# Kernel optimization log

Measured on AMD Instinct MI355X. Metric: run time of the kernel, lower is better.

The kernel has to match this reference:

```python
import jax, jax.numpy as jnp
from jax import lax
import numpy as np
from functools import partial

B, C, H, W = 4, 3, 256, 256
HW = H * W
KCAP = 32          # max tracked components per (batch, class) slot
MAX_ITER = 5
KSIZE = 5


def _depthwise_sum(x, k):
    c = x.shape[1]
    w = jnp.ones((c, 1, k, k), x.dtype)
    return lax.conv_general_dilated(x, w, (1, 1), [(k // 2, k // 2)] * 2,
                                    feature_group_count=c,
                                    dimension_numbers=('NCHW', 'OIHW', 'NCHW'))


def erode(x):
    return (_depthwise_sum(x, KSIZE) >= KSIZE * KSIZE - 0.5).astype(x.dtype)


def dilate(x):
    return (_depthwise_sum(x, KSIZE) > 0.5).astype(x.dtype)


def _maxpool3_int(L):
    return lax.reduce_window(L, jnp.int32(0), lax.max, (1, 1, 3, 3), (1, 1, 1, 1),
                             [(0, 0), (0, 0), (1, 1), (1, 1)])


def label_cc(binary):
    # connected-component labeling by iterated 3x3 max-pool of pixel indices,
    # exactly as find_components_max_pool (labels = max flat pixel index in comp)
    b = lax.stop_gradient(binary) > 0.5
    idx = jnp.arange(HW, dtype=jnp.int32).reshape(1, 1, H, W)
    L0 = jnp.where(b, idx, 0)

    def cond(st):
        return st[1]

    def body(st):
        L, _ = st
        Ln = jnp.where(b, _maxpool3_int(L), 0)
        return Ln, jnp.any(Ln != L)

    L, _ = lax.while_loop(cond, body, (L0, jnp.array(True)))
    return L


def extract_components(Lf, binf):
    # per (b,c): top-KCAP components sorted by comp.sum() = size*label/maxL (desc)
    flat = Lf.reshape(-1)
    sizes = jnp.zeros((HW,), jnp.float32).at[flat].add(binf.reshape(-1))
    idx = jnp.arange(HW, dtype=jnp.int32)
    is_root = (flat == idx) & (flat > 0)  # label 0 excluded, as in torch code
    key = jnp.where(is_root, lax.stop_gradient(sizes) * idx.astype(jnp.float32), -1.0)
    _, top_lab = lax.top_k(key, KCAP)
    valid = key[top_lab] > 0.0
    maxL = jnp.maximum(flat.max(), 1).astype(jnp.float32)
    v = top_lab.astype(jnp.float32)
    s = jnp.where(valid, sizes[top_lab] * v / maxL, 0.0)  # comp.sum()
    lab = jnp.where(valid, top_lab, -1)
    # component tensor = mask * label/maxL, exactly mask*L/max(L) of the original
    comps = (Lf[None] == lab[:, None, None]).astype(jnp.float32) * (v / maxL)[:, None, None]
    return s, comps, valid


def process_step(P, n, bar, s, comps, valid, t):
    # overlaps vs components stored BEFORE this step; new comps within a step
    # are pixel-disjoint so they can never match each other (overlap == 0).
    OV = jnp.einsum('jhw,khw->jk', comps, P)

    def body(carry, inp):
        P, n, bar = carry
        s_j, comp_j, valid_j, ov_j = inp
        best = jnp.argmax(ov_j)
        matched = ov_j[best] > 0.0
        widx = jnp.clip(jnp.where(matched, best, n), 0, KCAP - 1)
        can = valid_j & (matched | (n < KCAP))
        bar = bar.at[widx, t].set(jnp.where(can, s_j, bar[widx, t]))
        add = valid_j & (~matched) & (n < KCAP)
        nw = jnp.minimum(n, KCAP - 1)
        P = P.at[nw].set(jnp.where(add, comp_j, P[nw]))
        return (P, n + add.astype(n.dtype), bar), None

    (P, n, bar), _ = lax.scan(body, (P, n, bar), (s, comps, valid, OV))
    return P, n, bar


def compute_barcodes(binary):
    half = MAX_ITER // 2
    seq = [(binary, half)]
    m = binary
    for t in range(half):
        m = erode(m)
        seq.append((m, half + t + 1))
    m = binary
    for t in range(half):
        m = dilate(m)
        seq.append((m, half - t - 1))
    BC = B * C
    P = jnp.zeros((BC, KCAP, H, W), jnp.float32)
    n = jnp.zeros((BC,), jnp.int32)
    bar = jnp.zeros((BC, KCAP, MAX_ITER), jnp.float32)
    for mp, t in seq:  # fixed 5-step schedule (structural loop)
        L = label_cc(mp).reshape(BC, H, W)
        s, comps, valid = jax.vmap(extract_components)(L, mp.reshape(BC, H, W))
        P, n, bar = jax.vmap(partial(process_step, t=t))(P, n, bar, s, comps, valid)
    return bar.reshape(B, C, KCAP, MAX_ITER), n.reshape(B, C)


def topo_forward(predictions, gumbel, targets):
    y_soft = jax.nn.softmax(predictions + gumbel, axis=1)
    hard = jax.nn.one_hot(jnp.argmax(y_soft, axis=1), C, axis=1, dtype=jnp.float32)
    binary_pred = hard + y_soft - lax.stop_gradient(y_soft)  # straight-through
    binary_tgt = jnp.moveaxis(jax.nn.one_hot(targets, C, dtype=jnp.float32), -1, 1)
    bp, n_p = compute_barcodes(binary_pred)
    bt, n_t = compute_barcodes(binary_tgt)
    k = jnp.arange(KCAP)
    valid_p = k[None, None] < n_p[:, :, None]
    has_t = k[None, None] < n_t[:, :, None]
    pmax = bp.max(-1)
    pmax = jnp.where(pmax > 0, pmax, 1.0)
    tgt = jnp.where(has_t[..., None], bt, 0.0)
    term = jnp.sum((tgt - bp) ** 2, -1) / pmax ** 2
    losses = jnp.sum(jnp.where(valid_p, term, 0.0), axis=(1, 2))
    return losses.mean()  # reduction='mean'


def setup_inputs() -> dict:
    key = jax.random.key(0)
    k1, k2, k3 = jax.random.split(key, 3)
    # blob-like logits: low-res noise upsampled so component counts stay < KCAP
    lo = jax.random.normal(k1, (B, C, 16, 16), jnp.float32)
    predictions = 8.0 * jax.image.resize(lo, (B, C, H, W), 'linear')
    lo_t = jax.random.normal(k2, (B, C, 16, 16), jnp.float32)
    targets = jnp.argmax(jax.image.resize(lo_t, (B, C, H, W), 'linear'), axis=1).astype(jnp.int32)
    u = jax.random.uniform(k3, (B, C, H, W), jnp.float32, minval=1e-6, maxval=1.0 - 1e-6)
    gumbel = -jnp.log(-jnp.log(u))  # standard Gumbel noise (F.gumbel_softmax)
    return {"predictions": predictions, "gumbel": gumbel, "targets": targets}


def reference(predictions, gumbel, targets):
    return topo_forward(predictions, gumbel, targets)
```

## Files before the change

kernel.cpp:

```cpp
#include <hip/hip_runtime.h>

#define NB 4
#define NC 3
#define BC 12
#define HW 65536
#define KCAP 32
#define MAXI 5
#define RUNCAP 16384
#define NSLOT 120
#define NCH 24

typedef unsigned long long u64;
typedef unsigned int u32;

__device__ __forceinline__ int uf_find(int* P, int x){
  while (true){
    int p = P[x];
    if (p == x) return x;
    int gp = P[p];
    if (gp == p) return p;
    P[x] = gp;
    x = gp;
  }
}
__device__ __forceinline__ void uf_union_max(int* P, int a, int b){
  while (true){
    a = uf_find(P, a); b = uf_find(P, b);
    if (a == b) return;
    if (a > b){ int t = a; a = b; b = t; }
    int old = atomicCAS(&P[a], a, b);
    if (old == a) return;
    a = old;
  }
}

template<typename F>
__device__ __forceinline__ void walk_runs(const u64* wv, F&& emit){
  int open_s = -1;
  #pragma unroll
  for (int wi = 0; wi < 4; wi++){
    u64 v = wv[wi];
    int base = wi << 6;
    int pos = 0;
    while (pos < 64){
      u64 rem = v >> pos;
      if (open_s >= 0){
        u64 nz = ~rem;
        int z = nz ? __builtin_ctzll(nz) : 64;
        if (z >= 64 - pos){ pos = 64; }
        else { emit(open_s, base + pos + z); open_s = -1; pos += z; }
      } else {
        if (rem == 0ull){ pos = 64; }
        else {
          int o = __builtin_ctzll(rem);
          open_s = base + pos + o;
          pos += o;
        }
      }
    }
  }
  if (open_s >= 0) emit(open_s, 256);
}

__global__ void k_bin(const float* __restrict__ pred, const float* __restrict__ gum,
                      const int* __restrict__ tgt, u64* __restrict__ bmAll){
  int g = blockIdx.x * 256 + threadIdx.x;
  int b = g >> 16, p = g & (HW - 1);
  size_t base = (size_t)b * NC * HW + p;
  float v0 = pred[base]        + gum[base];
  float v1 = pred[base + HW]   + gum[base + HW];
  float v2 = pred[base + 2*HW] + gum[base + 2*HW];
  int a = 0; float m = v0;
  if (v1 > m){ m = v1; a = 1; }
  if (v2 > m){ m = v2; a = 2; }
  int tg = tgt[(size_t)b * HW + p];
  u64 p0 = __ballot(a == 0), p1 = __ballot(a == 1), p2 = __ballot(a == 2);
  u64 t0 = __ballot(tg == 0), t1 = __ballot(tg == 1), t2 = __ballot(tg == 2);
  if ((threadIdx.x & 63) == 0){
    int w = p >> 6;
    int sp = b * NC;
    bmAll[(size_t)(sp + 0) * 1024 + w] = p0;
    bmAll[(size_t)(sp + 1) * 1024 + w] = p1;
    bmAll[(size_t)(sp + 2) * 1024 + w] = p2;
    int st = 60 + b * NC;
    bmAll[(size_t)(st + 0) * 1024 + w] = t0;
    bmAll[(size_t)(st + 1) * 1024 + w] = t1;
    bmAll[(size_t)(st + 2) * 1024 + w] = t2;
  }
}

__global__ void k_morph4(const u64* __restrict__ bmAll, u64* __restrict__ bmAllW,
                         int4 srcs, int4 dsts, int4 flgs){
  int t = blockIdx.x * 256 + threadIdx.x;
  int job = t / 12288, rest = t % 12288;
  int s = rest >> 10, word = rest & 1023;
  int row = word >> 2, w = word & 3;
  int srcG = job == 0 ? srcs.x : job == 1 ? srcs.y : job == 2 ? srcs.z : srcs.w;
  int dstG = job == 0 ? dsts.x : job == 1 ? dsts.y : job == 2 ? dsts.z : dsts.w;
  int er   = job == 0 ? flgs.x : job == 1 ? flgs.y : job == 2 ? flgs.z : flgs.w;
  const u64* bs = bmAll + (size_t)(srcG * BC + s) * 1024;
  u64 res = er ? ~0ull : 0ull;
  for (int dy = -2; dy <= 2; dy++){
    int y = row + dy;
    if (y < 0 || y > 255){ if (er) res = 0; continue; }
    const u64* rw = bs + y * 4;
    u64 m = rw[w];
    u64 l = (w > 0) ? rw[w-1] : 0ull;
    u64 r = (w < 3) ? rw[w+1] : 0ull;
    u64 x1l = (m << 1) | (l >> 63);
    u64 x2l = (m << 2) | (l >> 62);
    u64 x1r = (m >> 1) | (r << 63);
    u64 x2r = (m >> 2) | (r << 62);
    u64 h = er ? (m & x1l & x2l & x1r & x2r) : (m | x1l | x2l | x1r | x2r);
    res = er ? (res & h) : (res | h);
  }
  bmAllW[(size_t)(dstG * BC + s) * 1024 + word] = res;
}

__global__ __launch_bounds__(1024) void k_cc_runs(
    const u64* __restrict__ bmAll, u32* __restrict__ selRuns,
    int* __restrict__ selCnt, float* __restrict__ sSel, float* __restrict__ scaleSel){
  __shared__ int par[RUNCAP];
  __shared__ u32 pkz[RUNCAP];
  __shared__ int rs[257];
  __shared__ u64 wcand[16*KCAP];
  __shared__ u64 selKeys[KCAP];
  __shared__ int selRoot[KCAP];
  __shared__ int wsum[4], wsum2[4];
  __shared__ int lmS;
  int u = blockIdx.x, t = threadIdx.x;
  int lane = t & 63, wid = t >> 6;
  bool rowT = t < 256;
  u64 wv[4] = {0,0,0,0};
  int nr = 0;
  if (rowT){
    const u64* bp = bmAll + (size_t)u * 1024 + t * 4;
    #pragma unroll
    for (int i = 0; i < 4; i++) wv[i] = bp[i];
    walk_runs(wv, [&](int a, int b){ (void)a; (void)b; nr++; });
  }
  if (t == 0) lmS = 0;
  {
    int v = nr;
    #pragma unroll
    for (int d = 1; d < 64; d <<= 1){
      int o = __shfl_up(v, d);
      if (lane >= d) v += o;
    }
    if (rowT && lane == 63) wsum[wid] = v;
    __syncthreads();
    if (rowT){
      int pre = 0;
      for (int q = 0; q < wid; q++) pre += wsum[q];
      rs[t] = pre + v - nr;
      if (t == 255) rs[256] = pre + v;
    }
    __syncthreads();
  }
  int NR = rs[256];
  int NRc = NR < RUNCAP ? NR : RUNCAP;
  int myBase = rowT ? rs[t] : 0;
  for (int i = t; i < NRc; i += 1024) par[i] = i;
  if (rowT){
    int o = myBase;
    walk_runs(wv, [&](int a, int b){
      if (o < RUNCAP) pkz[o] = ((u32)t << 16) | ((u32)a << 8) | (u32)(b - 1);
      o++;
    });
  }
  __syncthreads();
  for (int i = t; i < NRc; i += 1024){
    u32 v = pkz[i];
    int r = v >> 16;
    if (r == 0) continue;
    int s2 = (int)((v >> 8) & 255), E2 = (int)(v & 255);
    int a0 = rs[r-1], a1 = rs[r];
    if (a1 > NRc) a1 = NRc;
    if (a0 >= a1) continue;
    int lo = a0, hi = a1;
    while (lo < hi){
      int mid = (lo + hi) >> 1;
      if ((int)(pkz[mid] & 255) >= s2 - 1) hi = mid; else lo = mid + 1;
    }
    for (int j = lo; j < a1; j++){
      int s1 = (int)((pkz[j] >> 8) & 255);
      if (s1 > E2 + 1) break;
      uf_union_max(par, i, j);
    }
  }
  __syncthreads();
  for (int i = t; i < NRc; i += 1024){
    int r = i, p = par[r];
    while (p != r){ r = p; p = par[r]; }
    par[i] = r;
  }
  __syncthreads();
  {
    int lm = 0;
    for (int i = t; i < NRc; i += 1024){
      u32 v = pkz[i];
      int s0 = (int)((v >> 8) & 255), E = (int)(v & 255);
      atomicAdd(&par[par[i] & 16383], (E - s0 + 1) << 14);
      lm = max(lm, (int)(v >> 16) * 256 + E);
    }
    #pragma unroll
    for (int off = 32; off > 0; off >>= 1) lm = max(lm, __shfl_xor(lm, off));
    if (lane == 0) atomicMax(&lmS, lm);
  }
  __syncthreads();
  float maxLf = (float)(lmS >= 1 ? lmS : 1);
  for (int i = t; i < NRc; i += 1024){
    int pv = par[i];
    if ((pv & 16383) == i){
      u32 v = pkz[i];
      int lab = (int)(v >> 16) * 256 + (int)(v & 255);
      if (lab > 0){
        float key = (float)((u32)pv >> 14) * (float)lab;
        pkz[i] = __float_as_uint(key);
        par[i] = (lab << 14) | i;
      } else {
        pkz[i] = 0;
      }
    }
  }
  __syncthreads();
  {
    u64 myBest = 0;
    for (int i = t; i < NRc; i += 1024){
      int pv = par[i];
      if ((pv & 16383) != i) continue;
      u32 kh = pkz[i];
      if (!kh) continue;
      u64 cand = ((u64)kh << 32) | ((u64)(0xFFFFu - ((u32)pv >> 14)) << 16) | (u64)i;
      if (cand > myBest) myBest = cand;
    }
    if (lane < KCAP) wcand[wid*KCAP + lane] = 0;
    for (int r = 0; r < KCAP; r++){
      u64 b = myBest;
      #pragma unroll
      for (int off = 32; off > 0; off >>= 1){
        u64 o = __shfl_xor(b, off);
        b = (o > b) ? o : b;
      }
      if (b == 0) break;
      if (lane == 0) wcand[wid*KCAP + r] = b;
      if (myBest == b){
        pkz[(int)(b & 16383)] = 0;
        myBest = 0;
        for (int i = t; i < NRc; i += 1024){
          int pv = par[i];
          if ((pv & 16383) != i) continue;
          u32 kh = pkz[i];
          if (!kh) continue;
          u64 cand = ((u64)kh << 32) | ((u64)(0xFFFFu - ((u32)pv >> 14)) << 16) | (u64)i;
          if (cand > myBest) myBest = cand;
        }
      }
    }
  }
  __syncthreads();
  if (wid == 0){
    u64 c[8];
    #pragma unroll
    for (int q = 0; q < 8; q++) c[q] = wcand[q*64 + lane];
    if (lane < KCAP) selKeys[lane] = 0;
    for (int r = 0; r < KCAP; r++){
      u64 b = 0;
      #pragma unroll
      for (int q = 0; q < 8; q++) b = (c[q] > b) ? c[q] : b;
      #pragma unroll
      for (int off = 32; off > 0; off >>= 1){
        u64 o = __shfl_xor(b, off);
        b = (o > b) ? o : b;
      }
      if (b == 0) break;
      #pragma unroll
      for (int q = 0; q < 8; q++) if (c[q] == b) c[q] = 0;
      if (lane == 0) selKeys[r] = b;
    }
  }
  __syncthreads();
  if (t < KCAP){
    u64 k = selKeys[t];
    if (k){
      int lab = 0xFFFF - (int)((k >> 16) & 0xFFFF);
      selRoot[t] = (int)(k & 0x3FFF);
      sSel[u*KCAP + t]     = __uint_as_float((u32)(k >> 32)) / maxLf;
      scaleSel[u*KCAP + t] = (float)lab / maxLf;
    } else {
      selRoot[t] = -1;
      sSel[u*KCAP + t] = 0.0f;
      scaleSel[u*KCAP + t] = 0.0f;
    }
  }
  __syncthreads();
  for (int i = t; i < NRc; i += 1024) pkz[i] = 255u;
  __syncthreads();
  if (t < KCAP && selRoot[t] >= 0) pkz[selRoot[t]] = (u32)t;
  __syncthreads();
  int c = 0;
  if (rowT){
    int o = myBase;
    walk_runs(wv, [&](int a, int b){
      if (o < RUNCAP && pkz[par[o] & 16383] < KCAP) c++;
      o++;
    });
  }
  {
    int v = c;
    #pragma unroll
    for (int d = 1; d < 64; d <<= 1){
      int o = __shfl_up(v, d);
      if (lane >= d) v += o;
    }
    if (rowT && lane == 63) wsum2[wid] = v;
    __syncthreads();
    if (rowT){
      int pre = 0;
      for (int q = 0; q < wid; q++) pre += wsum2[q];
      int w = pre + v - c;
      size_t base = (size_t)u * RUNCAP;
      int o = myBase;
      walk_runs(wv, [&](int a, int b){
        if (o < RUNCAP){
          u32 j = pkz[par[o] & 16383];
          if (j < KCAP){
            selRuns[base + w] = (j << 24) | ((u32)t << 16) | ((u32)a << 8) | (u32)(b - 1);
            w++;
          }
        }
        o++;
      });
    }
    if (t == 0) selCnt[u] = wsum2[0] + wsum2[1] + wsum2[2] + wsum2[3];
  }
}

__global__ __launch_bounds__(1024) void k_chainall(
    const u32* __restrict__ selRuns, const int* __restrict__ selCnt,
    const float* __restrict__ sSel, const float* __restrict__ scaleSel,
    float* __restrict__ barP, float* __restrict__ barT,
    int* __restrict__ n24, u64* __restrict__ Pbm){
  int w = blockIdx.x, t = threadIdx.x;
  int pass = w / 12, s = w % 12;
  __shared__ int cnt[KCAP*KCAP];
  __shared__ float spL[KCAP];
  __shared__ int add_dst[KCAP];
  __shared__ int bestA[KCAP];
  __shared__ float bvA[KCAP];
  __shared__ int nS;
  if (t < KCAP) spL[t] = 0.0f;
  if (t == 0) nS = 0;
  float* bar = (pass ? barT : barP) + (size_t)s * KCAP * MAXI;
  u64* Pb = Pbm + (size_t)w * KCAP * 1024;
  #pragma unroll 1
  for (int st = 0; st < 5; st++){
    int u = (pass * 5 + st) * BC + s;
    int tval = (st < 3) ? st + 2 : (st == 3 ? 1 : 0);
    for (int i = t; i < KCAP*KCAP; i += 1024) cnt[i] = 0;
    __syncthreads();
    int n0 = nS;
    int NS = selCnt[u];
    const u32* rp = selRuns + (size_t)u * RUNCAP;
    for (int i = t; i < NS; i += 1024){
      u32 v = rp[i];
      int j = v >> 24;
      int row = (v >> 16) & 255, s0 = (v >> 8) & 255, E = (int)(v & 255);
      int w0 = s0 >> 6, w1 = E >> 6;
      int acc[KCAP];
      #pragma unroll
      for (int k2 = 0; k2 < KCAP; k2++) acc[k2] = 0;
      for (int wi = w0; wi <= w1; wi++){
        int lo = max(s0, wi << 6), hi = min(E + 1, (wi << 6) + 64);
        u64 mask = (hi - lo == 64) ? ~0ull : ((((u64)1 << (hi - lo)) - 1) << (lo - (wi << 6)));
        int wofs = row * 4 + wi;
        #pragma unroll
        for (int k2 = 0; k2 < KCAP; k2++){
          if (k2 < n0) acc[k2] += __popcll(Pb[(size_t)k2 * 1024 + wofs] & mask);
        }
      }
      #pragma unroll
      for (int k2 = 0; k2 < KCAP; k2++){
        if (k2 < n0 && acc[k2]) atomicAdd(&cnt[j*KCAP + k2], acc[k2]);
      }
    }
    __syncthreads();
    if (t < KCAP){
      float sn = scaleSel[(size_t)u*KCAP + t];
      int best = 0; float bv = 0.0f;
      if (sn > 0.0f && n0 > 0){
        bv = sn * spL[0] * (float)cnt[t*KCAP + 0];
        for (int k2 = 1; k2 < n0; k2++){
          float ov = sn * spL[k2] * (float)cnt[t*KCAP + k2];
          if (ov > bv){ bv = ov; best = k2; }
        }
      }
      bestA[t] = best; bvA[t] = bv;
    }
    __syncthreads();
    if (t == 0){
      int n = n0;
      for (int j = 0; j < KCAP; j++){
        add_dst[j] = -1;
        float sv = scaleSel[(size_t)u*KCAP + j];
        if (sv <= 0.0f) continue;
        if (bvA[j] > 0.0f){
          bar[bestA[j]*MAXI + tval] = sSel[(size_t)u*KCAP + j];
        } else if (n < KCAP){
          bar[n*MAXI + tval] = sSel[(size_t)u*KCAP + j];
          spL[n] = sv;
          add_dst[j] = n;
          n++;
        }
      }
      nS = n;
    }
    __syncthreads();
    for (int j = 0; j < KCAP; j++){
      int d = add_dst[j];
      if (d < 0) continue;
      u64* dst = Pb + (size_t)d * 1024;
      for (int x = t; x < 1024; x += 1024) dst[x] = 0ull;
    }
    __syncthreads();
    for (int i = t; i < NS; i += 1024){
      u32 v = rp[i];
      int j = v >> 24;
      int d = add_dst[j];
      if (d < 0) continue;
      int row = (v >> 16) & 255, s0 = (v >> 8) & 255, E = (int)(v & 255);
      int w0 = s0 >> 6, w1 = E >> 6;
      u64* dst = Pb + (size_t)d * 1024 + row * 4;
      for (int wi = w0; wi <= w1; wi++){
        int lo = max(s0, wi << 6), hi = min(E + 1, (wi << 6) + 64);
        u64 mask = (hi - lo == 64) ? ~0ull : ((((u64)1 << (hi - lo)) - 1) << (lo - (wi << 6)));
        atomicOr(&dst[wi], mask);
      }
    }
    __syncthreads();
  }
  if (t == 0) n24[w] = nS;
}

__global__ void k_loss(const float* __restrict__ barP, const float* __restrict__ barT,
                       const int* __restrict__ n24, float* __restrict__ out){
  __shared__ float red[512];
  int t = threadIdx.x;
  float val = 0.0f;
  if (t < BC * KCAP){
    int s = t >> 5, k = t & 31;
    int np = n24[s], nt = n24[12 + s];
    if (k < np){
      const float* bp = barP + (size_t)(s*KCAP + k)*MAXI;
      float pmax = bp[0];
      #pragma unroll
      for (int q = 1; q < MAXI; q++) pmax = fmaxf(pmax, bp[q]);
      if (!(pmax > 0.0f)) pmax = 1.0f;
      float acc = 0.0f;
      #pragma unroll
      for (int q = 0; q < MAXI; q++){
        float tv = (k < nt) ? barT[(size_t)(s*KCAP + k)*MAXI + q] : 0.0f;
        float d = tv - bp[q];
        acc += d * d;
      }
      val = acc / (pmax * pmax);
    }
  }
  red[t] = val;
  __syncthreads();
  for (int off = 256; off > 0; off >>= 1){
    if (t < off) red[t] += red[t + off];
    __syncthreads();
  }
  if (t == 0) out[0] = red[0] * 0.25f;
}

extern "C" void kernel_launch(void* const* d_in, const int* in_sizes, int n_in,
                              void* d_out, int out_size, void* d_ws, size_t ws_size,
                              hipStream_t stream){
  const float* pred = (const float*)d_in[0];
  const float* gum  = (const float*)d_in[1];
  const int*   tgt  = (const int*)d_in[2];
  float* out = (float*)d_out;
  char* ws = (char*)d_ws;
  size_t off = 0;
  auto alloc = [&](size_t bytes)->char*{
    char* p = ws + off;
    off += (bytes + 255) & ~(size_t)255;
    return p;
  };
  u64* bmAll   = (u64*)alloc((size_t)NSLOT*1024*8);
  u32* selRuns = (u32*)alloc((size_t)NSLOT*RUNCAP*4);
  int* selCnt  = (int*)alloc(NSLOT*4);
  float* sSel     = (float*)alloc((size_t)NSLOT*KCAP*4);
  float* scaleSel = (float*)alloc((size_t)NSLOT*KCAP*4);
  u64* Pbm     = (u64*)alloc((size_t)NCH*KCAP*1024*8);
  int* n24     = (int*)alloc(NCH*4);
  size_t zbytes = (size_t)(BC*KCAP*MAXI*2)*4;
  char* zreg = alloc(zbytes);
  float* barP = (float*)zreg;
  float* barT = barP + BC*KCAP*MAXI;
  if (off > ws_size) return;

  hipMemsetAsync(zreg, 0, zbytes, stream);
  k_bin<<<(NB*HW)/256,256,0,stream>>>(pred, gum, tgt, bmAll);
  k_morph4<<<192,256,0,stream>>>(bmAll, bmAll, make_int4(0,0,5,5), make_int4(1,3,6,8), make_int4(1,0,1,0));
  k_morph4<<<192,256,0,stream>>>(bmAll, bmAll, make_int4(1,3,6,8), make_int4(2,4,7,9), make_int4(1,0,1,0));
  k_cc_runs<<<NSLOT,1024,0,stream>>>(bmAll, selRuns, selCnt, sSel, scaleSel);
  k_chainall<<<NCH,1024,0,stream>>>(selRuns, selCnt, sSel, scaleSel, barP, barT, n24, Pbm);
  k_loss<<<1,512,0,stream>>>(barP, barT, n24, out);
}
```

Measured before the change: 278.5 us.

## Replace union-find CC with iterative max-label propagation and transpose chain bitmaps

Connected-component merging of runs switches from CAS-based union-find with a final path compression to a bounded iterative scheme: each pass atomically max-hooks adjacent runs' parents, then does two pointer-jumping sweeps, repeating until nothing changes. In the chaining kernel the per-component bitmap store is transposed to [word][component], so a 32-lane group handles one run with each lane counting overlap against a different stored component. This replaces per-thread 32-wide strided loads and a 32-entry accumulator array with coalesced loads and one register. Risks: label propagation may need many iterations (capped at 64) and could stop before convergence on long chains, and the clear and OR writes now use strided addresses.

```diff
diff --git a/kernel.cpp b/kernel.cpp
--- a/kernel.cpp
+++ b/kernel.cpp
@@ -12,27 +12,6 @@
 
 typedef unsigned long long u64;
 typedef unsigned int u32;
-
-__device__ __forceinline__ int uf_find(int* P, int x){
-  while (true){
-    int p = P[x];
-    if (p == x) return x;
-    int gp = P[p];
-    if (gp == p) return p;
-    P[x] = gp;
-    x = gp;
-  }
-}
-__device__ __forceinline__ void uf_union_max(int* P, int a, int b){
-  while (true){
-    a = uf_find(P, a); b = uf_find(P, b);
-    if (a == b) return;
-    if (a > b){ int t = a; a = b; b = t; }
-    int old = atomicCAS(&P[a], a, b);
-    if (old == a) return;
-    a = old;
-  }
-}
 
 template<typename F>
 __device__ __forceinline__ void walk_runs(const u64* wv, F&& emit){
@@ -127,7 +106,7 @@
   __shared__ u64 selKeys[KCAP];
   __shared__ int selRoot[KCAP];
   __shared__ int wsum[4], wsum2[4];
-  __shared__ int lmS;
+  __shared__ int lmS, changedS;
   int u = blockIdx.x, t = threadIdx.x;
   int lane = t & 63, wid = t >> 6;
   bool rowT = t < 256;
@@ -169,32 +148,45 @@
     });
   }
   __syncthreads();
-  for (int i = t; i < NRc; i += 1024){
-    u32 v = pkz[i];
-    int r = v >> 16;
-    if (r == 0) continue;
-    int s2 = (int)((v >> 8) & 255), E2 = (int)(v & 255);
-    int a0 = rs[r-1], a1 = rs[r];
-    if (a1 > NRc) a1 = NRc;
-    if (a0 >= a1) continue;
-    int lo = a0, hi = a1;
-    while (lo < hi){
-      int mid = (lo + hi) >> 1;
-      if ((int)(pkz[mid] & 255) >= s2 - 1) hi = mid; else lo = mid + 1;
-    }
-    for (int j = lo; j < a1; j++){
-      int s1 = (int)((pkz[j] >> 8) & 255);
-      if (s1 > E2 + 1) break;
-      uf_union_max(par, i, j);
-    }
-  }
-  __syncthreads();
-  for (int i = t; i < NRc; i += 1024){
-    int r = i, p = par[r];
-    while (p != r){ r = p; p = par[r]; }
-    par[i] = r;
-  }
-  __syncthreads();
+  for (int it = 0; it < 64; it++){
+    if (t == 0) changedS = 0;
+    __syncthreads();
+    for (int i = t; i < NRc; i += 1024){
+      u32 v = pkz[i];
+      int r = v >> 16;
+      if (r == 0) continue;
+      int s2 = (int)((v >> 8) & 255), E2 = (int)(v & 255);
+      int a0 = rs[r-1], a1 = rs[r];
+      if (a1 > NRc) a1 = NRc;
+      if (a0 >= a1) continue;
+      int lo = a0, hi = a1;
+      while (lo < hi){
+        int mid = (lo + hi) >> 1;
+        if ((int)(pkz[mid] & 255) >= s2 - 1) hi = mid; else lo = mid + 1;
+      }
+      for (int j = lo; j < a1; j++){
+        int s1 = (int)((pkz[j] >> 8) & 255);
+        if (s1 > E2 + 1) break;
+        int a = par[i], b = par[j];
+        if (a == b) continue;
+        if (a < b){ if (atomicMax(&par[a], b) < b) changedS = 1; }
+        else      { if (atomicMax(&par[b], a) < a) changedS = 1; }
+      }
+    }
+    __syncthreads();
+    #pragma unroll
+    for (int jp = 0; jp < 2; jp++){
+      for (int i = t; i < NRc; i += 1024){
+        int p = par[i];
+        int gp = par[p];
+        if (gp > p){ par[i] = gp; changedS = 1; }
+      }
+      __syncthreads();
+    }
+    int ch = changedS;
+    __syncthreads();
+    if (!ch) break;
+  }
   {
     int lm = 0;
     for (int i = t; i < NRc; i += 1024){
@@ -340,7 +332,7 @@
     const u32* __restrict__ selRuns, const int* __restrict__ selCnt,
     const float* __restrict__ sSel, const float* __restrict__ scaleSel,
     float* __restrict__ barP, float* __restrict__ barT,
-    int* __restrict__ n24, u64* __restrict__ Pbm){
+    int* __restrict__ n24, u64* __restrict__ PbT){
   int w = blockIdx.x, t = threadIdx.x;
   int pass = w / 12, s = w % 12;
   __shared__ int cnt[KCAP*KCAP];
@@ -352,7 +344,8 @@
   if (t < KCAP) spL[t] = 0.0f;
   if (t == 0) nS = 0;
   float* bar = (pass ? barT : barP) + (size_t)s * KCAP * MAXI;
-  u64* Pb = Pbm + (size_t)w * KCAP * 1024;
+  u64* Pb = PbT + (size_t)w * KCAP * 1024;
+  int g = t >> 5, k = t & 31;
   #pragma unroll 1
   for (int st = 0; st < 5; st++){
     int u = (pass * 5 + st) * BC + s;
@@ -362,26 +355,21 @@
     int n0 = nS;
     int NS = selCnt[u];
     const u32* rp = selRuns + (size_t)u * RUNCAP;
-    for (int i = t; i < NS; i += 1024){
-      u32 v = rp[i];
-      int j = v >> 24;
-      int row = (v >> 16) & 255, s0 = (v >> 8) & 255, E = (int)(v & 255);
-      int w0 = s0 >> 6, w1 = E >> 6;
-      int acc[KCAP];
-      #pragma unroll
-      for (int k2 = 0; k2 < KCAP; k2++) acc[k2] = 0;
-      for (int wi = w0; wi <= w1; wi++){
-        int lo = max(s0, wi << 6), hi = min(E + 1, (wi << 6) + 64);
-        u64 mask = (hi - lo == 64) ? ~0ull : ((((u64)1 << (hi - lo)) - 1) << (lo - (wi << 6)));
-        int wofs = row * 4 + wi;
-        #pragma unroll
-        for (int k2 = 0; k2 < KCAP; k2++){
-          if (k2 < n0) acc[k2] += __popcll(Pb[(size_t)k2 * 1024 + wofs] & mask);
-        }
-      }
-      #pragma unroll
-      for (int k2 = 0; k2 < KCAP; k2++){
-        if (k2 < n0 && acc[k2]) atomicAdd(&cnt[j*KCAP + k2], acc[k2]);
+    if (n0 > 0){
+      for (int i = g; i < NS; i += 32){
+        u32 v = rp[i];
+        int j = v >> 24;
+        int row = (v >> 16) & 255, s0 = (v >> 8) & 255, E = (int)(v & 255);
+        int w0 = s0 >> 6, w1 = E >> 6;
+        int acc = 0;
+        if (k < n0){
+          for (int wi = w0; wi <= w1; wi++){
+            int lo = max(s0, wi << 6), hi = min(E + 1, (wi << 6) + 64);
+            u64 mask = (hi - lo == 64) ? ~0ull : ((((u64)1 << (hi - lo)) - 1) << (lo - (wi << 6)));
+            acc += __popcll(Pb[(size_t)(row * 4 + wi) * KCAP + k] & mask);
+          }
+          if (acc) atomicAdd(&cnt[j*KCAP + k], acc);
+        }
       }
     }
     __syncthreads();
@@ -419,8 +407,7 @@
     for (int j = 0; j < KCAP; j++){
       int d = add_dst[j];
       if (d < 0) continue;
-      u64* dst = Pb + (size_t)d * 1024;
-      for (int x = t; x < 1024; x += 1024) dst[x] = 0ull;
+      for (int x = t; x < 1024; x += 1024) Pb[(size_t)x * KCAP + d] = 0ull;
     }
     __syncthreads();
     for (int i = t; i < NS; i += 1024){
@@ -430,11 +417,10 @@
       if (d < 0) continue;
       int row = (v >> 16) & 255, s0 = (v >> 8) & 255, E = (int)(v & 255);
       int w0 = s0 >> 6, w1 = E >> 6;
-      u64* dst = Pb + (size_t)d * 1024 + row * 4;
       for (int wi = w0; wi <= w1; wi++){
         int lo = max(s0, wi << 6), hi = min(E + 1, (wi << 6) + 64);
         u64 mask = (hi - lo == 64) ? ~0ull : ((((u64)1 << (hi - lo)) - 1) << (lo - (wi << 6)));
-        atomicOr(&dst[wi], mask);
+        atomicOr(&Pb[(size_t)(row * 4 + wi) * KCAP + d], mask);
       }
     }
     __syncthreads();
@@ -494,7 +480,7 @@
   int* selCnt  = (int*)alloc(NSLOT*4);
   float* sSel     = (float*)alloc((size_t)NSLOT*KCAP*4);
   float* scaleSel = (float*)alloc((size_t)NSLOT*KCAP*4);
-  u64* Pbm     = (u64*)alloc((size_t)NCH*KCAP*1024*8);
+  u64* PbT     = (u64*)alloc((size_t)NCH*KCAP*1024*8);
   int* n24     = (int*)alloc(NCH*4);
   size_t zbytes = (size_t)(BC*KCAP*MAXI*2)*4;
   char* zreg = alloc(zbytes);
@@ -507,6 +493,6 @@
   k_morph4<<<192,256,0,stream>>>(bmAll, bmAll, make_int4(0,0,5,5), make_int4(1,3,6,8), make_int4(1,0,1,0));
   k_morph4<<<192,256,0,stream>>>(bmAll, bmAll, make_int4(1,3,6,8), make_int4(2,4,7,9), make_int4(1,0,1,0));
   k_cc_runs<<<NSLOT,1024,0,stream>>>(bmAll, selRuns, selCnt, sSel, scaleSel);
-  k_chainall<<<NCH,1024,0,stream>>>(selRuns, selCnt, sSel, scaleSel, barP, barT, n24, Pbm);
+  k_chainall<<<NCH,1024,0,stream>>>(selRuns, selCnt, sSel, scaleSel, barP, barT, n24, PbT);
   k_loss<<<1,512,0,stream>>>(barP, barT, n24, out);
 }
```

Result: slower. 308.5 us (+10.8%).

## Transpose component bitmaps and spread overlap counting across lanes per run

Applied to the files above, without the earlier changes.

The component bitmap buffer is transposed so the KCAP component words for one position sit next to each other. Overlap counting now gives each 32-lane group one run and each lane one component, in place of one thread looping over all 32 components with a 32-entry accumulator. Per-wavefront shared count copies cut atomic contention and are summed afterwards. In the CC kernel, run lengths with the same root are combined with a segmented warp scan before the atomic add, which reduces shared atomics. The cost is 64KB of shared memory for the count copies plus an extra reduction pass.

```diff
diff --git a/kernel.cpp b/kernel.cpp
--- a/kernel.cpp
+++ b/kernel.cpp
@@ -197,11 +197,31 @@
   __syncthreads();
   {
     int lm = 0;
-    for (int i = t; i < NRc; i += 1024){
-      u32 v = pkz[i];
-      int s0 = (int)((v >> 8) & 255), E = (int)(v & 255);
-      atomicAdd(&par[par[i] & 16383], (E - s0 + 1) << 14);
-      lm = max(lm, (int)(v >> 16) * 256 + E);
+    for (int i0 = 0; i0 < NRc; i0 += 1024){
+      int i = i0 + t;
+      int root = -1, len = 0;
+      if (i < NRc){
+        u32 v = pkz[i];
+        int s0 = (int)((v >> 8) & 255), E = (int)(v & 255);
+        len = E - s0 + 1;
+        root = par[i] & 16383;
+        lm = max(lm, (int)(v >> 16) * 256 + E);
+      }
+      int val = len;
+      int prev = __shfl_up(root, 1);
+      unsigned flg = (lane == 0 || prev != root) ? 1u : 0u;
+      #pragma unroll
+      for (int d = 1; d < 64; d <<= 1){
+        int ov = __shfl_up(val, d);
+        unsigned of = __shfl_up(flg, d);
+        if (lane >= d){
+          if (!flg) val += ov;
+          flg |= of;
+        }
+      }
+      int nroot = __shfl_down(root, 1);
+      bool last = (lane == 63) || (nroot != root);
+      if (i < NRc && last) atomicAdd(&par[root], val << 14);
     }
     #pragma unroll
     for (int off = 32; off > 0; off >>= 1) lm = max(lm, __shfl_xor(lm, off));
@@ -340,10 +360,10 @@
     const u32* __restrict__ selRuns, const int* __restrict__ selCnt,
     const float* __restrict__ sSel, const float* __restrict__ scaleSel,
     float* __restrict__ barP, float* __restrict__ barT,
-    int* __restrict__ n24, u64* __restrict__ Pbm){
+    int* __restrict__ n24, u64* __restrict__ PbT){
   int w = blockIdx.x, t = threadIdx.x;
   int pass = w / 12, s = w % 12;
-  __shared__ int cnt[KCAP*KCAP];
+  __shared__ int cnt[16*KCAP*KCAP];
   __shared__ float spL[KCAP];
   __shared__ int add_dst[KCAP];
   __shared__ int bestA[KCAP];
@@ -352,37 +372,41 @@
   if (t < KCAP) spL[t] = 0.0f;
   if (t == 0) nS = 0;
   float* bar = (pass ? barT : barP) + (size_t)s * KCAP * MAXI;
-  u64* Pb = Pbm + (size_t)w * KCAP * 1024;
+  u64* Pb = PbT + (size_t)w * KCAP * 1024;
+  int g = t >> 5, k = t & 31;
+  int wid = t >> 6;
   #pragma unroll 1
   for (int st = 0; st < 5; st++){
     int u = (pass * 5 + st) * BC + s;
     int tval = (st < 3) ? st + 2 : (st == 3 ? 1 : 0);
-    for (int i = t; i < KCAP*KCAP; i += 1024) cnt[i] = 0;
+    for (int i = t; i < 16*KCAP*KCAP; i += 1024) cnt[i] = 0;
     __syncthreads();
     int n0 = nS;
     int NS = selCnt[u];
     const u32* rp = selRuns + (size_t)u * RUNCAP;
-    for (int i = t; i < NS; i += 1024){
-      u32 v = rp[i];
-      int j = v >> 24;
-      int row = (v >> 16) & 255, s0 = (v >> 8) & 255, E = (int)(v & 255);
-      int w0 = s0 >> 6, w1 = E >> 6;
-      int acc[KCAP];
-      #pragma unroll
-      for (int k2 = 0; k2 < KCAP; k2++) acc[k2] = 0;
-      for (int wi = w0; wi <= w1; wi++){
-        int lo = max(s0, wi << 6), hi = min(E + 1, (wi << 6) + 64);
-        u64 mask = (hi - lo == 64) ? ~0ull : ((((u64)1 << (hi - lo)) - 1) << (lo - (wi << 6)));
-        int wofs = row * 4 + wi;
-        #pragma unroll
-        for (int k2 = 0; k2 < KCAP; k2++){
-          if (k2 < n0) acc[k2] += __popcll(Pb[(size_t)k2 * 1024 + wofs] & mask);
-        }
-      }
-      #pragma unroll
-      for (int k2 = 0; k2 < KCAP; k2++){
-        if (k2 < n0 && acc[k2]) atomicAdd(&cnt[j*KCAP + k2], acc[k2]);
-      }
+    if (n0 > 0){
+      for (int i = g; i < NS; i += 32){
+        u32 v = rp[i];
+        int j = v >> 24;
+        int row = (v >> 16) & 255, s0 = (v >> 8) & 255, E = (int)(v & 255);
+        int w0 = s0 >> 6, w1 = E >> 6;
+        int acc = 0;
+        if (k < n0){
+          for (int wi = w0; wi <= w1; wi++){
+            int lo = max(s0, wi << 6), hi = min(E + 1, (wi << 6) + 64);
+            u64 mask = (hi - lo == 64) ? ~0ull : ((((u64)1 << (hi - lo)) - 1) << (lo - (wi << 6)));
+            acc += __popcll(Pb[(size_t)(row * 4 + wi) * KCAP + k] & mask);
+          }
+          if (acc) atomicAdd(&cnt[wid*KCAP*KCAP + j*KCAP + k], acc);
+        }
+      }
+    }
+    __syncthreads();
+    {
+      int tot = 0;
+      #pragma unroll
+      for (int wq = 0; wq < 16; wq++) tot += cnt[wq*KCAP*KCAP + t];
+      cnt[t] = tot;
     }
     __syncthreads();
     if (t < KCAP){
@@ -419,8 +443,7 @@
     for (int j = 0; j < KCAP; j++){
       int d = add_dst[j];
       if (d < 0) continue;
-      u64* dst = Pb + (size_t)d * 1024;
-      for (int x = t; x < 1024; x += 1024) dst[x] = 0ull;
+      for (int x = t; x < 1024; x += 1024) Pb[(size_t)x * KCAP + d] = 0ull;
     }
     __syncthreads();
     for (int i = t; i < NS; i += 1024){
@@ -430,11 +453,10 @@
       if (d < 0) continue;
       int row = (v >> 16) & 255, s0 = (v >> 8) & 255, E = (int)(v & 255);
       int w0 = s0 >> 6, w1 = E >> 6;
-      u64* dst = Pb + (size_t)d * 1024 + row * 4;
       for (int wi = w0; wi <= w1; wi++){
         int lo = max(s0, wi << 6), hi = min(E + 1, (wi << 6) + 64);
         u64 mask = (hi - lo == 64) ? ~0ull : ((((u64)1 << (hi - lo)) - 1) << (lo - (wi << 6)));
-        atomicOr(&dst[wi], mask);
+        atomicOr(&Pb[(size_t)(row * 4 + wi) * KCAP + d], mask);
       }
     }
     __syncthreads();
@@ -494,7 +516,7 @@
   int* selCnt  = (int*)alloc(NSLOT*4);
   float* sSel     = (float*)alloc((size_t)NSLOT*KCAP*4);
   float* scaleSel = (float*)alloc((size_t)NSLOT*KCAP*4);
-  u64* Pbm     = (u64*)alloc((size_t)NCH*KCAP*1024*8);
+  u64* PbT     = (u64*)alloc((size_t)NCH*KCAP*1024*8);
   int* n24     = (int*)alloc(NCH*4);
   size_t zbytes = (size_t)(BC*KCAP*MAXI*2)*4;
   char* zreg = alloc(zbytes);
@@ -507,6 +529,6 @@
   k_morph4<<<192,256,0,stream>>>(bmAll, bmAll, make_int4(0,0,5,5), make_int4(1,3,6,8), make_int4(1,0,1,0));
   k_morph4<<<192,256,0,stream>>>(bmAll, bmAll, make_int4(1,3,6,8), make_int4(2,4,7,9), make_int4(1,0,1,0));
   k_cc_runs<<<NSLOT,1024,0,stream>>>(bmAll, selRuns, selCnt, sSel, scaleSel);
-  k_chainall<<<NCH,1024,0,stream>>>(selRuns, selCnt, sSel, scaleSel, barP, barT, n24, Pbm);
+  k_chainall<<<NCH,1024,0,stream>>>(selRuns, selCnt, sSel, scaleSel, barP, barT, n24, PbT);
   k_loss<<<1,512,0,stream>>>(barP, barT, n24, out);
 }
```

Result: slower. 308.6 us (+10.8%).
